# Optimization experiments

Hardware: AMD Instinct MI355X
Metric: run time of the kernel (lower is better)

## Reference

```python
import jax, jax.numpy as jnp
import numpy as np

EMB = 256
N_NODES = 100000
N_EDGES = 500000
N_REL = 10
REL_DIM = 64
HID = 128
HEADS = 4
HEAD_DIM = HID // HEADS


def setup_inputs() -> dict:
    key = jax.random.key(0)
    ks = jax.random.split(key, 16)
    s = lambda i, shape: jax.random.normal(ks[i], shape, dtype=jnp.float32) * 0.05
    return {
        "node_embeddings": jax.random.normal(ks[0], (N_NODES, EMB), dtype=jnp.float32),
        "edge_index": jax.random.randint(ks[1], (2, N_EDGES), 0, N_NODES),
        "relation_type": jax.random.randint(ks[2], (N_EDGES,), 0, N_REL),
        "rel_emb": s(3, (N_REL, REL_DIM)),
        "W_edge": s(4, (2 * EMB, HID)), "b_edge": jnp.zeros((HID,), jnp.float32),
        "W_q": s(5, (REL_DIM, HID)), "b_q": jnp.zeros((HID,), jnp.float32),
        "W_k": s(6, (HID, HID)), "b_k": jnp.zeros((HID,), jnp.float32),
        "W_v": s(7, (HID, HID)), "b_v": jnp.zeros((HID,), jnp.float32),
        "W_o1": s(8, (HID, HID)), "b_o1": jnp.zeros((HID,), jnp.float32),
        "W_o2": s(9, (HID, 1)), "b_o2": jnp.zeros((1,), jnp.float32),
    }


def reference(node_embeddings, edge_index, relation_type, rel_emb,
              W_edge, b_edge, W_q, b_q, W_k, b_k, W_v, b_v,
              W_o1, b_o1, W_o2, b_o2):
    # Gather endpoint features: [E, 2*EMB]
    src = node_embeddings[edge_index[0]]
    tgt = node_embeddings[edge_index[1]]
    edge_features = jnp.concatenate([src, tgt], axis=1)
    # Edge MLP (dropout is identity at eval): [E, HID]
    edge_hidden = jax.nn.relu(edge_features @ W_edge + b_edge)
    # Relation embedding lookup: [E, REL_DIM]
    rel = rel_emb[relation_type]
    E = edge_hidden.shape[0]
    Q = (rel @ W_q + b_q).reshape(E, HEADS, HEAD_DIM)
    K = (edge_hidden @ W_k + b_k).reshape(E, HEADS, HEAD_DIM)
    V = (edge_hidden @ W_v + b_v).reshape(E, HEADS, HEAD_DIM)
    scale = jnp.sqrt(jnp.float32(HEAD_DIM))
    scores = jnp.sum(Q * K, axis=-1) / scale          # [E, HEADS]
    attn = jax.nn.softmax(scores, axis=-1)            # softmax over heads
    attended = (attn[..., None] * V).reshape(E, HID)
    output = attended + edge_hidden
    # Output MLP: Linear->ReLU->Linear(1)
    h = jax.nn.relu(output @ W_o1 + b_o1)
    score = (h @ W_o2 + b_o2).squeeze(-1)             # [E]
    return score
```

## Files before the change

### kernel.cpp

```cpp
#include <hip/hip_runtime.h>

#define EMB   256
#define HID   128
#define RELD  64
#define NREL  10
#define TE    128
#define SHSTR 130

typedef __attribute__((ext_vector_type(8)))  short bf16x8;
typedef __attribute__((ext_vector_type(16))) float f32x16;

__device__ __forceinline__ float bf16_to_f32(unsigned short u) {
    union { unsigned int i; float f; } v;
    v.i = ((unsigned int)u) << 16;
    return v.f;
}

__device__ __forceinline__ unsigned short f32_to_bf16(float x) {
    union { unsigned int i; float f; } v;
    v.f = x;
    unsigned int b = v.i;
    unsigned int rounded = b + 0x7fffu + ((b >> 16) & 1u);
    return (unsigned short)(rounded >> 16);
}

template <bool F32>
__device__ __forceinline__ float ldx(const void* p, size_t i) {
    if (F32) return ((const float*)p)[i];
    return bf16_to_f32(((const unsigned short*)p)[i]);
}

__device__ __forceinline__ bool detect_f32(const void* nodeEmb) {
    const float* f = (const float*)nodeEmb;
    float x = f[(threadIdx.x & 63) * 997];
    bool sane = isfinite(x) && fabsf(x) < 1.0e6f;
    unsigned long long m = __ballot(sane);
    return __popcll(m) >= 48;
}

__device__ __forceinline__ void gload16(const void* g, void* l) {
    __builtin_amdgcn_global_load_lds(
        (const __attribute__((address_space(1))) unsigned int*)g,
        (__attribute__((address_space(3))) unsigned int*)l, 16, 0, 0);
}

#define WAITVL(n) asm volatile("s_waitcnt vmcnt(" #n ") lgkmcnt(0)" ::: "memory")

__device__ __forceinline__ void sbar() {
    __builtin_amdgcn_sched_barrier(0);
    __builtin_amdgcn_s_barrier();
    __builtin_amdgcn_sched_barrier(0);
}
__device__ __forceinline__ void bar_lds() {
    asm volatile("s_waitcnt lgkmcnt(0)" ::: "memory");
    sbar();
}

template <bool F32>
__device__ void prep_body(int vb, const void* W_edge, const void* W_k,
                          const void* W_v, const void* W_o1, const void* rel_emb,
                          const void* W_q, const void* b_q,
                          unsigned short* WTe, unsigned short* WTk,
                          unsigned short* WTv, unsigned short* WTo1, float* Qtab)
{
    if (vb < 448) {
        int idx = vb * 256 + threadIdx.x;
        if (idx < 65536) {
            int kc = idx >> 12, e = idx & 4095;
            int g = e >> 3, j = e & 7;
            int col = g & 127, kg = g >> 7;
            int k = kc * 32 + kg * 8 + j;
            WTe[idx] = f32_to_bf16(ldx<F32>(W_edge, (size_t)k * HID + col));
        } else if (idx < 65536 + 16384) {
            int i = idx - 65536;
            int kc = i >> 12, e = i & 4095;
            int g = e >> 3, j = e & 7;
            int col = g & 127, kg = (g >> 7) & 3;
            int k = kc * 32 + kg * 8 + j;
            WTk[i] = f32_to_bf16(ldx<F32>(W_k, (size_t)k * HID + col));
        } else if (idx < 65536 + 2 * 16384) {
            int i = idx - 65536 - 16384;
            int kc = i >> 12, e = i & 4095;
            int g = e >> 3, j = e & 7;
            int col = g & 127, kg = (g >> 7) & 3;
            int k = kc * 32 + kg * 8 + j;
            WTv[i] = f32_to_bf16(ldx<F32>(W_v, (size_t)k * HID + col));
        } else {
            int i = idx - 65536 - 2 * 16384;
            int kc = i >> 12, e = i & 4095;
            int g = e >> 3, j = e & 7;
            int col = g & 127, kg = (g >> 7) & 3;
            int k = kc * 32 + kg * 8 + j;
            WTo1[i] = f32_to_bf16(ldx<F32>(W_o1, (size_t)k * HID + col));
        }
    } else {
        const int t = threadIdx.x;
        const int c = t & (HID - 1);
        const int h = t >> 7;
        for (int r = h; r < NREL; r += 2) {
            float acc = 0.f;
            for (int d = 0; d < RELD; ++d)
                acc += ldx<F32>(rel_emb, r * RELD + d) * ldx<F32>(W_q, (size_t)d * HID + c);
            Qtab[r * HID + c] = acc + ldx<F32>(b_q, c);
        }
    }
}

__global__ void prep_kernel(const void* nodeEmb,
                            const void* W_edge, const void* W_k, const void* W_v,
                            const void* W_o1, const void* rel_emb, const void* W_q,
                            const void* b_q,
                            unsigned short* WTe, unsigned short* WTk,
                            unsigned short* WTv, unsigned short* WTo1, float* Qtab,
                            unsigned short* nodeBf16, int convBlocks,
                            unsigned long long nodeElems)
{
    bool f32 = detect_f32(nodeEmb);
    int b = blockIdx.x;
    if (b < convBlocks) {
        if (!f32) return;
        unsigned long long i = (unsigned long long)b * 2048ull + threadIdx.x * 8;
        if (i + 8 <= nodeElems) {
            const float* src = (const float*)nodeEmb + i;
            float4 f0 = *(const float4*)src;
            float4 f1 = *(const float4*)(src + 4);
            union { unsigned short us[8]; uint4 v; } pk;
            pk.us[0] = f32_to_bf16(f0.x); pk.us[1] = f32_to_bf16(f0.y);
            pk.us[2] = f32_to_bf16(f0.z); pk.us[3] = f32_to_bf16(f0.w);
            pk.us[4] = f32_to_bf16(f1.x); pk.us[5] = f32_to_bf16(f1.y);
            pk.us[6] = f32_to_bf16(f1.z); pk.us[7] = f32_to_bf16(f1.w);
            *(uint4*)(nodeBf16 + i) = pk.v;
        }
        return;
    }
    b -= convBlocks;
    if (f32) prep_body<true >(b, W_edge, W_k, W_v, W_o1, rel_emb, W_q, b_q,
                              WTe, WTk, WTv, WTo1, Qtab);
    else     prep_body<false>(b, W_edge, W_k, W_v, W_o1, rel_emb, W_q, b_q,
                              WTe, WTk, WTv, WTo1, Qtab);
}

struct __align__(16) Smem {
    unsigned short sHid[16 * SHSTR * 8];
    unsigned short SB[2][4096];
    float sQf[NREL * HID];
    float sBias[5 * HID];
    float sSc[TE][4];
    float sAttn[TE][4];
    float sPart[TE][2];
    int   sSrc[TE], sTgt[TE], sRel[TE];
};

__device__ __forceinline__ int shid_idx(int row, int k) {
    return (((k >> 3) * SHSTR + row) << 3) + (k & 7);
}

template <bool GBF16>
__device__ __forceinline__ bf16x8 loadA8(const void* row, int off) {
    if (GBF16) {
        return *(const bf16x8*)((const unsigned short*)row + off);
    } else {
        const float* p = (const float*)row + off;
        float4 f0 = *(const float4*)p;
        float4 f1 = *(const float4*)(p + 4);
        union { unsigned short us[8]; bf16x8 v; } pk;
        pk.us[0] = f32_to_bf16(f0.x); pk.us[1] = f32_to_bf16(f0.y);
        pk.us[2] = f32_to_bf16(f0.z); pk.us[3] = f32_to_bf16(f0.w);
        pk.us[4] = f32_to_bf16(f1.x); pk.us[5] = f32_to_bf16(f1.y);
        pk.us[6] = f32_to_bf16(f1.z); pk.us[7] = f32_to_bf16(f1.w);
        return pk.v;
    }
}

template <bool F32, bool GBF16>
__device__ void fused_body(
    Smem& sm,
    const void* gsrc, const int* edgeIdx, const int* relType,
    const unsigned short* WTe, const unsigned short* WTk,
    const unsigned short* WTv, const unsigned short* WTo1,
    const void* b_edge, const void* b_k, const void* b_v,
    const void* b_o1, const void* W_o2, const void* b_o2,
    const float* Qtab, void* outp, int E)
{
    const int t   = threadIdx.x;
    const int l   = t & 63;
    const int w   = t >> 6;
    const int c   = l & 31;
    const int h5  = l >> 5;
    const int rt  = w >> 1;
    const int cg2 = w & 1;
    const int bs  = blockIdx.x * TE;
    const int aRow = 32 * rt + c;

    if (t < TE) {
        int e = bs + t;
        if (e >= E) e = E - 1;
        if (e < 0)  e = 0;
        sm.sSrc[t] = edgeIdx[e];
        sm.sTgt[t] = edgeIdx[E + e];
        int r = relType[e];
        if (r < 0) r = 0;
        if (r >= NREL) r = NREL - 1;
        sm.sRel[t] = r;
    }
    for (int i = t; i < 5 * HID; i += 512) {
        int which = i >> 7, j = i & (HID - 1);
        float v = (which == 0) ? ldx<F32>(b_edge, j)
                : (which == 1) ? ldx<F32>(b_k, j)
                : (which == 2) ? ldx<F32>(b_v, j)
                : (which == 3) ? ldx<F32>(b_o1, j)
                               : ldx<F32>(W_o2, j);
        sm.sBias[i] = v;
    }
    for (int i = t; i < NREL * HID; i += 512)
        sm.sQf[i] = Qtab[i];
    __syncthreads();

    const void* rowSrc;
    const void* rowTgt;
    if (GBF16) {
        rowSrc = (const void*)((const unsigned short*)gsrc + (size_t)sm.sSrc[aRow] * EMB);
        rowTgt = (const void*)((const unsigned short*)gsrc + (size_t)sm.sTgt[aRow] * EMB);
    } else {
        rowSrc = (const void*)((const float*)gsrc + (size_t)sm.sSrc[aRow] * EMB);
        rowTgt = (const void*)((const float*)gsrc + (size_t)sm.sTgt[aRow] * EMB);
    }

    char* const ldsWaveB0 = (char*)sm.SB[0] + w * 1024;
    char* const ldsWaveB1 = (char*)sm.SB[1] + w * 1024;

    #define LOAD_A(kc, s) \
        loadA8<GBF16>(((kc) < 8) ? rowSrc : rowTgt, ((kc) & 7) * 32 + (s) * 16 + h5 * 8)
    #define STAGE_B(WT, kc, buf)                                                 \
        gload16((WT) + (kc) * 4096 + t * 8, (buf) ? ldsWaveB1 : ldsWaveB0);

    #define MFMA_AR(slot, buf, accv)                                             \
    {                                                                            \
        const char* sb_ = (const char*)sm.SB[(buf)];                             \
        _Pragma("unroll")                                                        \
        for (int s_ = 0; s_ < 2; ++s_) {                                         \
            _Pragma("unroll")                                                    \
            for (int ct_ = 0; ct_ < 2; ++ct_) {                                  \
                bf16x8 b_ = *(const bf16x8*)                                     \
                    (sb_ + ((s_ * 256 + h5 * 128 + 64 * cg2 + 32 * ct_ + c) << 4)); \
                accv[ct_] = __builtin_amdgcn_mfma_f32_32x32x16_bf16(             \
                                aR[slot][s_], b_, accv[ct_], 0, 0, 0);           \
            }                                                                    \
        }                                                                        \
    }

    #define MFMA_H(kc, buf, accv)                                                \
    {                                                                            \
        const char* sb_ = (const char*)sm.SB[(buf)];                             \
        _Pragma("unroll")                                                        \
        for (int s_ = 0; s_ < 2; ++s_) {                                         \
            bf16x8 a_ = *(const bf16x8*)((const char*)sm.sHid +                  \
                         ((((kc) * 4 + s_ * 2 + h5) * SHSTR + aRow) << 4));      \
            _Pragma("unroll")                                                    \
            for (int ct_ = 0; ct_ < 2; ++ct_) {                                  \
                bf16x8 b_ = *(const bf16x8*)                                     \
                    (sb_ + ((s_ * 256 + h5 * 128 + 64 * cg2 + 32 * ct_ + c) << 4)); \
                accv[ct_] = __builtin_amdgcn_mfma_f32_32x32x16_bf16(             \
                                a_, b_, accv[ct_], 0, 0, 0);                     \
            }                                                                    \
        }                                                                        \
    }

    f32x16 acc[2];
    acc[0] = (f32x16)(0.0f); acc[1] = (f32x16)(0.0f);
    {
        bf16x8 aR[4][2];
        #pragma unroll
        for (int p = 0; p < 3; ++p) {
            aR[p][0] = LOAD_A(p, 0);
            aR[p][1] = LOAD_A(p, 1);
        }
        STAGE_B(WTe, 0, 0);
        STAGE_B(WTe, 1, 1);
        #pragma unroll
        for (int kc = 0; kc < 16; ++kc) {
            int buf = kc & 1;
            if (kc == 0)      { WAITVL(1); }
            else if (kc < 14) { WAITVL(3); }
            else if (kc == 14){ WAITVL(1); }
            else              { WAITVL(0); }
            sbar();
            MFMA_AR((kc & 3), buf, acc);
            sbar();
            if (kc < 13) {
                aR[(kc + 3) & 3][0] = LOAD_A(kc + 3, 0);
                aR[(kc + 3) & 3][1] = LOAD_A(kc + 3, 1);
            }
            if (kc < 14) STAGE_B(WTe, kc + 2, buf);
        }
    }
    STAGE_B(WTk, 0, 0); STAGE_B(WTk, 1, 1);
    {
        #pragma unroll
        for (int ct = 0; ct < 2; ++ct) {
            int col = 64 * cg2 + 32 * ct + c;
            float bb = sm.sBias[col];
            #pragma unroll
            for (int r = 0; r < 16; ++r) {
                int erow = 32 * rt + (r & 3) + 8 * (r >> 2) + 4 * h5;
                sm.sHid[shid_idx(erow, col)] = f32_to_bf16(fmaxf(acc[ct][r] + bb, 0.f));
            }
        }
    }
    bar_lds();

    f32x16 kacc[2];
    kacc[0] = (f32x16)(0.0f); kacc[1] = (f32x16)(0.0f);
    #pragma unroll
    for (int kc = 0; kc < 4; ++kc) {
        int buf = kc & 1;
        if (kc < 3) { WAITVL(1); } else { WAITVL(0); }
        sbar();
        MFMA_H(kc, buf, kacc);
        sbar();
        if (kc < 2) STAGE_B(WTk, kc + 2, buf);
    }
    STAGE_B(WTv, 0, 0); STAGE_B(WTv, 1, 1);

    {
        float ps[2][16];
        #pragma unroll
        for (int ct = 0; ct < 2; ++ct) {
            int col = 64 * cg2 + 32 * ct + c;
            float bk = sm.sBias[HID + col];
            #pragma unroll
            for (int r = 0; r < 16; ++r) {
                int erow = 32 * rt + (r & 3) + 8 * (r >> 2) + 4 * h5;
                ps[ct][r] = (kacc[ct][r] + bk) * sm.sQf[sm.sRel[erow] * HID + col];
            }
        }
        #pragma unroll
        for (int m = 1; m < 32; m <<= 1)
            #pragma unroll
            for (int ct = 0; ct < 2; ++ct)
                #pragma unroll
                for (int r = 0; r < 16; ++r)
                    ps[ct][r] += __shfl_xor(ps[ct][r], m, 64);
        if (c == 0) {
            const float inv = 0.17677669529663687f;
            #pragma unroll
            for (int ct = 0; ct < 2; ++ct) {
                int head = 2 * cg2 + ct;
                #pragma unroll
                for (int r = 0; r < 16; ++r) {
                    int erow = 32 * rt + (r & 3) + 8 * (r >> 2) + 4 * h5;
                    sm.sSc[erow][head] = ps[ct][r] * inv;
                }
            }
        }
    }
    bar_lds();
    if (t < TE) {
        float s0 = sm.sSc[t][0], s1 = sm.sSc[t][1];
        float s2 = sm.sSc[t][2], s3 = sm.sSc[t][3];
        float m = fmaxf(fmaxf(s0, s1), fmaxf(s2, s3));
        float e0 = expf(s0 - m), e1 = expf(s1 - m);
        float e2 = expf(s2 - m), e3 = expf(s3 - m);
        float den = e0 + e1 + e2 + e3;
        sm.sAttn[t][0] = e0 / den; sm.sAttn[t][1] = e1 / den;
        sm.sAttn[t][2] = e2 / den; sm.sAttn[t][3] = e3 / den;
    }
    bar_lds();

    f32x16 vacc[2];
    vacc[0] = (f32x16)(0.0f); vacc[1] = (f32x16)(0.0f);
    #pragma unroll
    for (int kc = 0; kc < 4; ++kc) {
        int buf = kc & 1;
        if (kc < 3) { WAITVL(1); } else { WAITVL(0); }
        sbar();
        MFMA_H(kc, buf, vacc);
        sbar();
        if (kc < 2) STAGE_B(WTv, kc + 2, buf);
    }
    STAGE_B(WTo1, 0, 0); STAGE_B(WTo1, 1, 1);

    {
        #pragma unroll
        for (int ct = 0; ct < 2; ++ct) {
            int col  = 64 * cg2 + 32 * ct + c;
            int head = 2 * cg2 + ct;
            float bv = sm.sBias[2 * HID + col];
            #pragma unroll
            for (int r = 0; r < 16; ++r) {
                int erow = 32 * rt + (r & 3) + 8 * (r >> 2) + 4 * h5;
                float at = sm.sAttn[erow][head];
                int   si = shid_idx(erow, col);
                float hv = bf16_to_f32(sm.sHid[si]);
                sm.sHid[si] = f32_to_bf16(at * (vacc[ct][r] + bv) + hv);
            }
        }
    }
    bar_lds();

    f32x16 oacc[2];
    oacc[0] = (f32x16)(0.0f); oacc[1] = (f32x16)(0.0f);
    #pragma unroll
    for (int kc = 0; kc < 4; ++kc) {
        int buf = kc & 1;
        if (kc < 3) { WAITVL(1); } else { WAITVL(0); }
        sbar();
        MFMA_H(kc, buf, oacc);
        sbar();
        if (kc < 2) STAGE_B(WTo1, kc + 2, buf);
    }
    {
        float pr[16];
        #pragma unroll
        for (int r = 0; r < 16; ++r) pr[r] = 0.f;
        #pragma unroll
        for (int ct = 0; ct < 2; ++ct) {
            int col = 64 * cg2 + 32 * ct + c;
            float bo = sm.sBias[3 * HID + col];
            float wo = sm.sBias[4 * HID + col];
            #pragma unroll
            for (int r = 0; r < 16; ++r)
                pr[r] += fmaxf(oacc[ct][r] + bo, 0.f) * wo;
        }
        #pragma unroll
        for (int m = 1; m < 32; m <<= 1)
            #pragma unroll
            for (int r = 0; r < 16; ++r)
                pr[r] += __shfl_xor(pr[r], m, 64);
        if (c == 0) {
            #pragma unroll
            for (int r = 0; r < 16; ++r) {
                int erow = 32 * rt + (r & 3) + 8 * (r >> 2) + 4 * h5;
                sm.sPart[erow][cg2] = pr[r];
            }
        }
    }
    bar_lds();
    if (t < TE) {
        int ge = bs + t;
        if (ge < E) {
            float val = sm.sPart[t][0] + sm.sPart[t][1] + ldx<F32>(b_o2, 0);
            if (F32) ((float*)outp)[ge] = val;
            else     ((unsigned short*)outp)[ge] = f32_to_bf16(val);
        }
    }

    #undef LOAD_A
    #undef STAGE_B
    #undef MFMA_AR
    #undef MFMA_H
}

__global__ __launch_bounds__(512, 4) void RelationAttentionMLPHead_10539849744626_kernel(
    const void* nodeEmb, const unsigned short* nodeBf16, int useConv,
    const int* edgeIdx, const int* relType,
    const unsigned short* WTe, const unsigned short* WTk,
    const unsigned short* WTv, const unsigned short* WTo1,
    const void* b_edge, const void* b_k, const void* b_v,
    const void* b_o1, const void* W_o2, const void* b_o2,
    const float* Qtab, void* outp, int E)
{
    __shared__ Smem sm;
    if (detect_f32(nodeEmb)) {
        if (useConv)
            fused_body<true, true >(sm, nodeBf16, edgeIdx, relType, WTe, WTk, WTv, WTo1,
                                    b_edge, b_k, b_v, b_o1, W_o2, b_o2, Qtab, outp, E);
        else
            fused_body<true, false>(sm, nodeEmb, edgeIdx, relType, WTe, WTk, WTv, WTo1,
                                    b_edge, b_k, b_v, b_o1, W_o2, b_o2, Qtab, outp, E);
    } else {
        fused_body<false, true>(sm, nodeEmb, edgeIdx, relType, WTe, WTk, WTv, WTo1,
                                b_edge, b_k, b_v, b_o1, W_o2, b_o2, Qtab, outp, E);
    }
}

extern "C" void kernel_launch(void* const* d_in, const int* in_sizes, int n_in,
                              void* d_out, int out_size, void* d_ws, size_t ws_size,
                              hipStream_t stream) {
    (void)n_in;

    const void* nodeEmb = d_in[0];
    const int*  edgeIdx = (const int*)d_in[1];
    const int*  relType = (const int*)d_in[2];
    const void* rel_emb = d_in[3];
    const void* W_edge  = d_in[4];
    const void* b_edge  = d_in[5];
    const void* W_q     = d_in[6];
    const void* b_q     = d_in[7];
    const void* W_k     = d_in[8];
    const void* b_k     = d_in[9];
    const void* W_v     = d_in[10];
    const void* b_v     = d_in[11];
    const void* W_o1    = d_in[12];
    const void* b_o1    = d_in[13];
    const void* W_o2    = d_in[14];
    const void* b_o2    = d_in[15];

    int E = out_size;
    if (E <= 0) E = in_sizes ? in_sizes[2] : 0;
    if (E <= 0) E = 500000;

    unsigned long long nodeElems =
        (in_sizes && in_sizes[0] > 0) ? (unsigned long long)in_sizes[0] : 25600000ull;

    char* ws = (char*)d_ws;
    float*          Qtab     = (float*)ws;
    unsigned short* WTe      = (unsigned short*)(ws + 8192);
    unsigned short* WTk      = (unsigned short*)(ws + 139264);
    unsigned short* WTv      = (unsigned short*)(ws + 172032);
    unsigned short* WTo1     = (unsigned short*)(ws + 204800);
    unsigned short* nodeBf16 = (unsigned short*)(ws + 237568);

    size_t need = 237568ull + nodeElems * 2ull;
    int useConv = (ws_size >= need) ? 1 : 0;
    int convBlocks = useConv ? (int)((nodeElems + 2047ull) / 2048ull) : 0;

    prep_kernel<<<convBlocks + 449, 256, 0, stream>>>(
        nodeEmb, W_edge, W_k, W_v, W_o1, rel_emb, W_q, b_q,
        WTe, WTk, WTv, WTo1, Qtab, nodeBf16, convBlocks, nodeElems);

    int grid = (E + TE - 1) / TE;
    if (grid < 1) grid = 1;

    RelationAttentionMLPHead_10539849744626_kernel<<<grid, 512, 0, stream>>>(
        nodeEmb, nodeBf16, useConv, edgeIdx, relType, WTe, WTk, WTv, WTo1,
        b_edge, b_k, b_v, b_o1, W_o2, b_o2, Qtab, d_out, E);
}
```

Measured before the change: 428.3 us.

## Double K-chunk size to 64 in staged MFMA pipeline, halving barrier count

Each pipeline stage now stages two 32-wide weight chunks into a doubled LDS B buffer and issues twice as many MFMAs between barriers. The edge-MLP loop drops from 16 to 8 iterations and the K/V/O1 GEMMs from 4 to 2, halving the number of s_barrier/waitcnt synchronisations. The cost is double the LDS for B tiles, which may reduce occupancy. The fp32-input path now waits fully on every iteration, giving up load/compute overlap there.

```diff
diff --git a/kernel.cpp b/kernel.cpp
--- a/kernel.cpp
+++ b/kernel.cpp
@@ -142,7 +142,7 @@
 
 struct __align__(16) Smem {
     unsigned short sHid[16 * SHSTR * 8];
-    unsigned short SB[2][4096];
+    unsigned short SB[2][8192];
     float sQf[NREL * HID];
     float sBias[5 * HID];
     float sSc[TE][4];
@@ -226,75 +226,93 @@
         rowTgt = (const void*)((const float*)gsrc + (size_t)sm.sTgt[aRow] * EMB);
     }
 
-    char* const ldsWaveB0 = (char*)sm.SB[0] + w * 1024;
-    char* const ldsWaveB1 = (char*)sm.SB[1] + w * 1024;
-
-    #define LOAD_A(kc, s) \
-        loadA8<GBF16>(((kc) < 8) ? rowSrc : rowTgt, ((kc) & 7) * 32 + (s) * 16 + h5 * 8)
-    #define STAGE_B(WT, kc, buf)                                                 \
-        gload16((WT) + (kc) * 4096 + t * 8, (buf) ? ldsWaveB1 : ldsWaveB0);
-
-    #define MFMA_AR(slot, buf, accv)                                             \
+    char* const ldsB0 = (char*)sm.SB[0] + w * 1024;
+    char* const ldsB1 = (char*)sm.SB[1] + w * 1024;
+
+    #define LOAD_A(k32, s) \
+        loadA8<GBF16>(((k32) < 8) ? rowSrc : rowTgt, ((k32) & 7) * 32 + (s) * 16 + h5 * 8)
+    #define STAGE_B64(WT, kc, buf)                                               \
+    {                                                                            \
+        gload16((WT) + (2 * (kc)    ) * 4096 + t * 8,                            \
+                ((buf) ? ldsB1 : ldsB0));                                        \
+        gload16((WT) + (2 * (kc) + 1) * 4096 + t * 8,                            \
+                ((buf) ? ldsB1 : ldsB0) + 8192);                                 \
+    }
+
+    #define MFMA_AR64(slot, buf, accv)                                           \
     {                                                                            \
         const char* sb_ = (const char*)sm.SB[(buf)];                             \
+        _Pragma("unroll")                                                        \
+        for (int h_ = 0; h_ < 2; ++h_)                                           \
         _Pragma("unroll")                                                        \
         for (int s_ = 0; s_ < 2; ++s_) {                                         \
             _Pragma("unroll")                                                    \
             for (int ct_ = 0; ct_ < 2; ++ct_) {                                  \
                 bf16x8 b_ = *(const bf16x8*)                                     \
-                    (sb_ + ((s_ * 256 + h5 * 128 + 64 * cg2 + 32 * ct_ + c) << 4)); \
+                    (sb_ + h_ * 8192 +                                           \
+                     ((s_ * 256 + h5 * 128 + 64 * cg2 + 32 * ct_ + c) << 4));    \
                 accv[ct_] = __builtin_amdgcn_mfma_f32_32x32x16_bf16(             \
-                                aR[slot][s_], b_, accv[ct_], 0, 0, 0);           \
+                                aR[slot][h_ * 2 + s_], b_, accv[ct_], 0, 0, 0);  \
             }                                                                    \
         }                                                                        \
     }
 
-    #define MFMA_H(kc, buf, accv)                                                \
+    #define MFMA_H64(kc, buf, accv)                                              \
     {                                                                            \
         const char* sb_ = (const char*)sm.SB[(buf)];                             \
         _Pragma("unroll")                                                        \
+        for (int h_ = 0; h_ < 2; ++h_)                                           \
+        _Pragma("unroll")                                                        \
         for (int s_ = 0; s_ < 2; ++s_) {                                         \
             bf16x8 a_ = *(const bf16x8*)((const char*)sm.sHid +                  \
-                         ((((kc) * 4 + s_ * 2 + h5) * SHSTR + aRow) << 4));      \
+                ((((2 * (kc) + h_) * 4 + s_ * 2 + h5) * SHSTR + aRow) << 4));    \
             _Pragma("unroll")                                                    \
             for (int ct_ = 0; ct_ < 2; ++ct_) {                                  \
                 bf16x8 b_ = *(const bf16x8*)                                     \
-                    (sb_ + ((s_ * 256 + h5 * 128 + 64 * cg2 + 32 * ct_ + c) << 4)); \
+                    (sb_ + h_ * 8192 +                                           \
+                     ((s_ * 256 + h5 * 128 + 64 * cg2 + 32 * ct_ + c) << 4));    \
                 accv[ct_] = __builtin_amdgcn_mfma_f32_32x32x16_bf16(             \
                                 a_, b_, accv[ct_], 0, 0, 0);                     \
             }                                                                    \
         }                                                                        \
     }
 
+    #define FILL_A(slot, kc)                                                     \
+    {                                                                            \
+        aR[slot][0] = LOAD_A(2 * (kc),     0);                                   \
+        aR[slot][1] = LOAD_A(2 * (kc),     1);                                   \
+        aR[slot][2] = LOAD_A(2 * (kc) + 1, 0);                                   \
+        aR[slot][3] = LOAD_A(2 * (kc) + 1, 1);                                   \
+    }
+
     f32x16 acc[2];
     acc[0] = (f32x16)(0.0f); acc[1] = (f32x16)(0.0f);
     {
-        bf16x8 aR[4][2];
-        #pragma unroll
-        for (int p = 0; p < 3; ++p) {
-            aR[p][0] = LOAD_A(p, 0);
-            aR[p][1] = LOAD_A(p, 1);
-        }
-        STAGE_B(WTe, 0, 0);
-        STAGE_B(WTe, 1, 1);
-        #pragma unroll
-        for (int kc = 0; kc < 16; ++kc) {
+        bf16x8 aR[2][4];
+        FILL_A(0, 0);
+        FILL_A(1, 1);
+        STAGE_B64(WTe, 0, 0);
+        STAGE_B64(WTe, 1, 1);
+        #pragma unroll
+        for (int kc = 0; kc < 8; ++kc) {
             int buf = kc & 1;
-            if (kc == 0)      { WAITVL(1); }
-            else if (kc < 14) { WAITVL(3); }
-            else if (kc == 14){ WAITVL(1); }
-            else              { WAITVL(0); }
+            if (GBF16) {
+                if (kc == 0)      { WAITVL(2); }
+                else if (kc < 7)  { WAITVL(6); }
+                else              { WAITVL(0); }
+            } else {
+                WAITVL(0);
+            }
             sbar();
-            MFMA_AR((kc & 3), buf, acc);
+            MFMA_AR64((kc & 1), buf, acc);
             sbar();
-            if (kc < 13) {
-                aR[(kc + 3) & 3][0] = LOAD_A(kc + 3, 0);
-                aR[(kc + 3) & 3][1] = LOAD_A(kc + 3, 1);
-            }
-            if (kc < 14) STAGE_B(WTe, kc + 2, buf);
-        }
-    }
-    STAGE_B(WTk, 0, 0); STAGE_B(WTk, 1, 1);
+            if (kc < 6) {
+                FILL_A((kc & 1), kc + 2);
+                STAGE_B64(WTe, kc + 2, buf);
+            }
+        }
+    }
+    STAGE_B64(WTk, 0, 0); STAGE_B64(WTk, 1, 1);
     {
         #pragma unroll
         for (int ct = 0; ct < 2; ++ct) {
@@ -311,16 +329,14 @@
 
     f32x16 kacc[2];
     kacc[0] = (f32x16)(0.0f); kacc[1] = (f32x16)(0.0f);
-    #pragma unroll
-    for (int kc = 0; kc < 4; ++kc) {
-        int buf = kc & 1;
-        if (kc < 3) { WAITVL(1); } else { WAITVL(0); }
-        sbar();
-        MFMA_H(kc, buf, kacc);
-        sbar();
-        if (kc < 2) STAGE_B(WTk, kc + 2, buf);
-    }
-    STAGE_B(WTv, 0, 0); STAGE_B(WTv, 1, 1);
+    WAITVL(2); sbar();
+    MFMA_H64(0, 0, kacc);
+    sbar();
+    STAGE_B64(WTv, 0, 0);
+    WAITVL(2); sbar();
+    MFMA_H64(1, 1, kacc);
+    sbar();
+    STAGE_B64(WTv, 1, 1);
 
     {
         float ps[2][16];
@@ -369,16 +385,14 @@
 
     f32x16 vacc[2];
     vacc[0] = (f32x16)(0.0f); vacc[1] = (f32x16)(0.0f);
-    #pragma unroll
-    for (int kc = 0; kc < 4; ++kc) {
-        int buf = kc & 1;
-        if (kc < 3) { WAITVL(1); } else { WAITVL(0); }
-        sbar();
-        MFMA_H(kc, buf, vacc);
-        sbar();
-        if (kc < 2) STAGE_B(WTv, kc + 2, buf);
-    }
-    STAGE_B(WTo1, 0, 0); STAGE_B(WTo1, 1, 1);
+    WAITVL(2); sbar();
+    MFMA_H64(0, 0, vacc);
+    sbar();
+    STAGE_B64(WTo1, 0, 0);
+    WAITVL(2); sbar();
+    MFMA_H64(1, 1, vacc);
+    sbar();
+    STAGE_B64(WTo1, 1, 1);
 
     {
         #pragma unroll
@@ -400,15 +414,12 @@
 
     f32x16 oacc[2];
     oacc[0] = (f32x16)(0.0f); oacc[1] = (f32x16)(0.0f);
-    #pragma unroll
-    for (int kc = 0; kc < 4; ++kc) {
-        int buf = kc & 1;
-        if (kc < 3) { WAITVL(1); } else { WAITVL(0); }
-        sbar();
-        MFMA_H(kc, buf, oacc);
-        sbar();
-        if (kc < 2) STAGE_B(WTo1, kc + 2, buf);
-    }
+    WAITVL(2); sbar();
+    MFMA_H64(0, 0, oacc);
+    sbar();
+    WAITVL(0); sbar();
+    MFMA_H64(1, 1, oacc);
+    sbar();
     {
         float pr[16];
         #pragma unroll
@@ -446,9 +457,10 @@
     }
 
     #undef LOAD_A
-    #undef STAGE_B
-    #undef MFMA_AR
-    #undef MFMA_H
+    #undef STAGE_B64
+    #undef MFMA_AR64
+    #undef MFMA_H64
+    #undef FILL_A
 }
 
 __global__ __launch_bounds__(512, 4) void RelationAttentionMLPHead_10539849744626_kernel(
```

After: 429.3 us. Within noise of the previous version (+0.2%).
